# Performance work log

Measured on AMD Instinct MI355X. Metric: run time of the kernel, lower is better.

The kernel has to match this reference:

```python
import jax, jax.numpy as jnp
import numpy as np

P = 1024
D_FF = 4096
TGT = 4096
SRC = 4096


def _ln(x, g, b, eps=1e-5):
    mu = jnp.mean(x, axis=-1, keepdims=True)
    var = jnp.mean((x - mu) ** 2, axis=-1, keepdims=True)
    return (x - mu) / jnp.sqrt(var + eps) * g + b


def setup_inputs() -> dict:
    key = jax.random.key(0)
    ks = jax.random.split(key, 32)
    s = 1.0 / np.sqrt(P)
    sf = 1.0 / np.sqrt(D_FF)
    d = {
        "Y": jax.random.normal(ks[0], (TGT, P), jnp.float32),
        "Xp": jax.random.normal(ks[1], (SRC, P), jnp.float32),
        # self-attn projections (Linear: y = x @ W + b, W stored [in, out])
        "wq1": jax.random.uniform(ks[2], (P, P), jnp.float32, -s, s),
        "bq1": jnp.zeros((P,), jnp.float32),
        "wk1": jax.random.uniform(ks[3], (P, P), jnp.float32, -s, s),
        "bk1": jnp.zeros((P,), jnp.float32),
        "wv1": jax.random.uniform(ks[4], (P, P), jnp.float32, -s, s),
        "bv1": jnp.zeros((P,), jnp.float32),
        "w0": jax.random.uniform(ks[5], (P, P), jnp.float32, -s, s),
        "b0": jnp.zeros((P,), jnp.float32),
        "g1": jnp.ones((P,), jnp.float32),
        "be1": jnp.zeros((P,), jnp.float32),
        # cross-attn projections
        "wq2": jax.random.uniform(ks[6], (P, P), jnp.float32, -s, s),
        "bq2": jnp.zeros((P,), jnp.float32),
        "wk2": jax.random.uniform(ks[7], (P, P), jnp.float32, -s, s),
        "bk2": jnp.zeros((P,), jnp.float32),
        "wv2": jax.random.uniform(ks[8], (P, P), jnp.float32, -s, s),
        "bv2": jnp.zeros((P,), jnp.float32),
        "w1": jax.random.uniform(ks[9], (P, P), jnp.float32, -s, s),
        "b1": jnp.zeros((P,), jnp.float32),
        "g2": jnp.ones((P,), jnp.float32),
        "be2": jnp.zeros((P,), jnp.float32),
        # FFN
        "w2": jax.random.uniform(ks[10], (P, D_FF), jnp.float32, -s, s),
        "b2": jnp.zeros((D_FF,), jnp.float32),
        "w3": jax.random.uniform(ks[11], (D_FF, P), jnp.float32, -sf, sf),
        "b3": jnp.zeros((P,), jnp.float32),
        "g3": jnp.ones((P,), jnp.float32),
        "be3": jnp.zeros((P,), jnp.float32),
    }
    return d


def reference(Y, Xp, wq1, bq1, wk1, bk1, wv1, bv1, w0, b0, g1, be1,
              wq2, bq2, wk2, bk2, wv2, bv2, w1, b1, g2, be2,
              w2, b2, w3, b3, g3, be3):
    m = Y.shape[0]
    scale = 1.0 / jnp.sqrt(jnp.asarray(P, Y.dtype))
    # --- masked self-attention on Y ---
    Q = Y @ wq1 + bq1            # [m, p]
    K = Y @ wk1 + bk1
    V = Y @ wv1 + bv1
    S = (Q @ K.T) * scale        # [m, m]
    causal = jnp.tril(jnp.ones((m, m), bool))
    S = jnp.where(causal, S, jnp.asarray(-1e9, S.dtype))
    A = jax.nn.softmax(S, axis=-1)
    T1 = (A @ V) @ w0 + b0
    U1 = _ln(Y + T1, g1, be1)
    # --- cross-attention with encoder output Xp ---
    Q = U1 @ wq2 + bq2           # [m, p]
    K = Xp @ wk2 + bk2           # [n, p]
    V = Xp @ wv2 + bv2
    S = (Q @ K.T) * scale        # [m, n]
    A = jax.nn.softmax(S, axis=-1)
    T2 = (A @ V) @ w1 + b1
    U2 = _ln(U1 + T2, g2, be2)
    # --- position-wise FFN ---
    Z = jax.nn.relu(U2 @ w2 + b2) @ w3 + b3
    U3 = _ln(U2 + Z, g3, be3)
    return U3
```

## Files before the change

kernel.cpp:

```cpp
#include <hip/hip_runtime.h>
#include <hip/hip_bf16.h>

typedef __bf16 bf16x8 __attribute__((ext_vector_type(8)));
typedef __bf16 bf16x4 __attribute__((ext_vector_type(4)));
typedef float f32x4 __attribute__((ext_vector_type(4)));

#define AS1P(p) ((__attribute__((address_space(1))) void*)(void*)(p))
#define AS3P(p) ((__attribute__((address_space(3))) void*)(p))

__global__ __launch_bounds__(256, 3) void gemm_bt(
    const __hip_bfloat16* __restrict__ A, int lda,
    const __hip_bfloat16* __restrict__ Bt, int ldb,
    int M, int N, int K, int ldc,
    const float* __restrict__ bias, int bias_mode,
    float scale,
    const float* __restrict__ residual,
    int relu, int causal_skip, int trapezoid, int ksplit,
    float* __restrict__ Cf, __hip_bfloat16* __restrict__ Cb,
    int vcol0, __hip_bfloat16* __restrict__ Vt, int ldvt,
    int nsplit1, const __hip_bfloat16* __restrict__ A2,
    const __hip_bfloat16* __restrict__ Bt2, int ldb2, int ldc2,
    const float* __restrict__ bias2, __hip_bfloat16* __restrict__ Cb2,
    int vcol0_2, __hip_bfloat16* __restrict__ Vt2, int ldvt2)
{
    int nb = blockIdx.x;
    int mb = blockIdx.y;
    {
        const int gx = gridDim.x, gy = gridDim.y;
        if ((gx & 3) == 0 && (gy & 1) == 0) {
            const int id = mb * gx + nb;
            const int X  = id & 7;
            const int L  = id >> 3;
            const int rn = gx >> 2, rm = gy >> 1;
            const int nb_l = L / rm, mb_l = L - nb_l * rm;
            nb = (X & 3) * rn + nb_l;
            mb = (X >> 2) * rm + mb_l;
        }
    }
    if (nsplit1 && nb >= nsplit1) {
        A = A2; Bt = Bt2; ldb = ldb2; ldc = ldc2; bias = bias2;
        Cb = Cb2; Cf = nullptr; residual = nullptr;
        vcol0 = vcol0_2; Vt = Vt2; ldvt = ldvt2;
        nb -= nsplit1;
    }
    const int m_base = mb * 128;
    const int n_base = nb * 128;
    if (causal_skip && (n_base > m_base + 127)) return;
    int Kend = K;
    if (trapezoid) { int kl = m_base + 128; Kend = kl < K ? kl : K; }
    int kb = 0, ke = Kend;
    if (ksplit) {
        kb = blockIdx.z * ksplit;
        int k2 = kb + ksplit; ke = k2 < Kend ? k2 : Kend;
        if (kb >= ke) return;
        Cb += (size_t)blockIdx.z * M * ldc;
        Cf = nullptr;
    }
    const int nt = (ke - kb) >> 5;

    __shared__ __align__(16) __hip_bfloat16 Lds[3][8192];

    const int tid  = threadIdx.x;
    const int lane = tid & 63;
    const int wave = tid >> 6;
    const int wm = (wave >> 1) * 64;
    const int wn = (wave & 1) * 64;

    f32x4 acc[4][4];
#pragma unroll
    for (int i = 0; i < 4; ++i)
#pragma unroll
        for (int j = 0; j < 4; ++j) acc[i][j] = f32x4{0.f, 0.f, 0.f, 0.f};

    const bool isA = wave < 2;
    const __hip_bfloat16* G = isA ? (A + (size_t)m_base * lda) : (Bt + (size_t)n_base * ldb);
    const int ldg = isA ? lda : ldb;
    const int q0 = (wave & 1) * 4;
    const int rsub = lane >> 2;
    const int cx   = (lane & 3) ^ ((lane >> 3) & 3);
    const size_t grow = (size_t)(q0 * 16 + rsub) * ldg + (size_t)cx * 8 + kb;
    const int ldsoff = (isA ? 0 : 4096) + q0 * 512;

    const int lrow = lane & 15;
    const int cph  = ((lane >> 4) ^ ((lrow >> 1) & 3)) * 8;

#define ISSUE_TILE(KT, STG)                                                      \
    {                                                                            \
        const __hip_bfloat16* g = G + grow + (size_t)(KT) * 32;                  \
        __hip_bfloat16* dst = &Lds[STG][ldsoff];                                 \
        _Pragma("unroll")                                                        \
        for (int q = 0; q < 4; ++q) {                                            \
            __builtin_amdgcn_global_load_lds(AS1P(g), AS3P(dst), 16, 0, 0);      \
            g += (size_t)16 * ldg; dst += 512;                                   \
        }                                                                        \
    }

    ISSUE_TILE(0, 0)
    if (nt > 1) ISSUE_TILE(1, 1)

    int cur = 0;
    for (int kt = 0; kt < nt; ++kt) {
        __builtin_amdgcn_sched_barrier(0);
        if (kt + 1 < nt) __builtin_amdgcn_s_waitcnt(0x0F74);
        else             __builtin_amdgcn_s_waitcnt(0x0F70);
        __builtin_amdgcn_sched_barrier(0);
        __builtin_amdgcn_s_barrier();
        __builtin_amdgcn_sched_barrier(0);
        if (kt + 2 < nt) {
            int s2 = cur + 2; if (s2 >= 3) s2 -= 3;
            ISSUE_TILE(kt + 2, s2)
        }

        bf16x8 af[4], bfv[4];
#pragma unroll
        for (int i = 0; i < 4; ++i)
            af[i] = *(const bf16x8*)&Lds[cur][(wm + i * 16 + lrow) * 32 + cph];
#pragma unroll
        for (int j = 0; j < 4; ++j)
            bfv[j] = *(const bf16x8*)&Lds[cur][4096 + (wn + j * 16 + lrow) * 32 + cph];
#pragma unroll
        for (int i = 0; i < 4; ++i)
#pragma unroll
            for (int j = 0; j < 4; ++j)
                acc[i][j] = __builtin_amdgcn_mfma_f32_16x16x32_bf16(af[i], bfv[j], acc[i][j], 0, 0, 0);

        cur = (cur + 1 == 3) ? 0 : cur + 1;
    }
#undef ISSUE_TILE

    const int r0 = (lane >> 4) * 4;
    const int c0 = lane & 15;
    const bool vtrans = (n_base >= vcol0);
#pragma unroll
    for (int i = 0; i < 4; ++i) {
#pragma unroll
        for (int j = 0; j < 4; ++j) {
            const int col = n_base + wn + j * 16 + c0;
            const int row0 = m_base + wm + i * 16 + r0;
            float vv[4];
#pragma unroll
            for (int r = 0; r < 4; ++r) {
                float v = acc[i][j][r] * scale;
                if (bias_mode == 1) v += bias[col];
                else if (bias_mode == 2) v += bias[row0 + r];
                if (relu) v = fmaxf(v, 0.f);
                vv[r] = v;
            }
            if (vtrans) {
                bf16x4 o = { (__bf16)vv[0], (__bf16)vv[1], (__bf16)vv[2], (__bf16)vv[3] };
                *(bf16x4*)(Vt + (size_t)(col - vcol0) * ldvt + row0) = o;
            } else {
#pragma unroll
                for (int r = 0; r < 4; ++r) {
                    const size_t idx = (size_t)(row0 + r) * ldc + col;
                    float v = vv[r];
                    if (residual) v += residual[idx];
                    if (Cf) Cf[idx] = v;
                    else    Cb[idx] = __float2bfloat16(v);
                }
            }
        }
    }
}

__global__ __launch_bounds__(256, 2) void gemm_bt2(
    const __hip_bfloat16* __restrict__ A, int lda,
    const __hip_bfloat16* __restrict__ Bt, int ldb,
    int M, int N, int K, int ldc,
    const float* __restrict__ bias, int bias_mode,
    float scale,
    int relu, int causal_skip, int trapezoid, int ksplit,
    __hip_bfloat16* __restrict__ Cb)
{
    int nb = blockIdx.x;
    int mb = blockIdx.y;
    {
        const int gx = gridDim.x, gy = gridDim.y;
        if ((gx & 3) == 0 && (gy & 1) == 0) {
            const int id = mb * gx + nb;
            const int X  = id & 7;
            const int L  = id >> 3;
            const int rn = gx >> 2, rm = gy >> 1;
            const int nb_l = L / rm, mb_l = L - nb_l * rm;
            nb = (X & 3) * rn + nb_l;
            mb = (X >> 2) * rm + mb_l;
        }
    }
    const int m_base = mb * 256;
    const int n_base = nb * 128;
    if (causal_skip && (n_base > m_base + 255)) return;
    int Kend = K;
    if (trapezoid) { int kl = m_base + 256; Kend = kl < K ? kl : K; }
    int kb = 0, ke = Kend;
    if (ksplit) {
        kb = blockIdx.z * ksplit;
        int k2 = kb + ksplit; ke = k2 < Kend ? k2 : Kend;
        if (kb >= ke) return;
        Cb += (size_t)blockIdx.z * M * ldc;
    }
    const int nt = (ke - kb) >> 5;

    __shared__ __align__(16) __hip_bfloat16 Lds[3][12288];

    const int tid  = threadIdx.x;
    const int lane = tid & 63;
    const int wave = tid >> 6;
    const int wtm = (wave >> 1) * 128;
    const int wtn = (wave & 1) * 64;

    f32x4 acc[8][4];
#pragma unroll
    for (int i = 0; i < 8; ++i)
#pragma unroll
        for (int j = 0; j < 4; ++j) acc[i][j] = f32x4{0.f, 0.f, 0.f, 0.f};

    const int rsub = lane >> 2;
    const int cx   = (lane & 3) ^ ((lane >> 3) & 3);
    const __hip_bfloat16* GA = A  + (size_t)(m_base + wave * 64) * lda + (size_t)rsub * lda + (size_t)cx * 8 + kb;
    const __hip_bfloat16* GB = Bt + (size_t)(n_base + wave * 32) * ldb + (size_t)rsub * ldb + (size_t)cx * 8 + kb;
    const int ldsA = wave * 2048;
    const int ldsB = 8192 + wave * 1024;

    const int lrow = lane & 15;
    const int cph  = ((lane >> 4) ^ ((lrow >> 1) & 3)) * 8;

#define ISSUE_TILE2(KT, STG)                                                     \
    {                                                                            \
        const size_t ko = (size_t)(KT) * 32;                                     \
        const __hip_bfloat16* ga = GA + ko;                                      \
        __hip_bfloat16* da = &Lds[STG][ldsA];                                    \
        _Pragma("unroll")                                                        \
        for (int q = 0; q < 4; ++q) {                                            \
            __builtin_amdgcn_global_load_lds(AS1P(ga), AS3P(da), 16, 0, 0);      \
            ga += (size_t)16 * lda; da += 512;                                   \
        }                                                                        \
        const __hip_bfloat16* gb = GB + ko;                                      \
        __hip_bfloat16* db = &Lds[STG][ldsB];                                    \
        _Pragma("unroll")                                                        \
        for (int q = 0; q < 2; ++q) {                                            \
            __builtin_amdgcn_global_load_lds(AS1P(gb), AS3P(db), 16, 0, 0);      \
            gb += (size_t)16 * ldb; db += 512;                                   \
        }                                                                        \
    }

    ISSUE_TILE2(0, 0)
    if (nt > 1) ISSUE_TILE2(1, 1)

    int cur = 0;
    for (int kt = 0; kt < nt; ++kt) {
        __builtin_amdgcn_sched_barrier(0);
        if (kt + 1 < nt) __builtin_amdgcn_s_waitcnt(0x0F76);
        else             __builtin_amdgcn_s_waitcnt(0x0F70);
        __builtin_amdgcn_sched_barrier(0);
        __builtin_amdgcn_s_barrier();
        __builtin_amdgcn_sched_barrier(0);
        if (kt + 2 < nt) {
            int s2 = cur + 2; if (s2 >= 3) s2 -= 3;
            ISSUE_TILE2(kt + 2, s2)
        }

        bf16x8 af[8], bfv[4];
#pragma unroll
        for (int i = 0; i < 8; ++i)
            af[i] = *(const bf16x8*)&Lds[cur][(wtm + i * 16 + lrow) * 32 + cph];
#pragma unroll
        for (int j = 0; j < 4; ++j)
            bfv[j] = *(const bf16x8*)&Lds[cur][8192 + (wtn + j * 16 + lrow) * 32 + cph];
#pragma unroll
        for (int i = 0; i < 8; ++i)
#pragma unroll
            for (int j = 0; j < 4; ++j)
                acc[i][j] = __builtin_amdgcn_mfma_f32_16x16x32_bf16(af[i], bfv[j], acc[i][j], 0, 0, 0);

        cur = (cur + 1 == 3) ? 0 : cur + 1;
    }
#undef ISSUE_TILE2

    const int r0 = (lane >> 4) * 4;
    const int c0 = lane & 15;
#pragma unroll
    for (int i = 0; i < 8; ++i) {
#pragma unroll
        for (int j = 0; j < 4; ++j) {
            const int col = n_base + wtn + j * 16 + c0;
#pragma unroll
            for (int r = 0; r < 4; ++r) {
                const int row = m_base + wtm + i * 16 + r0 + r;
                float v = acc[i][j][r] * scale;
                if (bias_mode == 1) v += bias[col];
                else if (bias_mode == 2) v += bias[row];
                if (relu) v = fmaxf(v, 0.f);
                Cb[(size_t)row * ldc + col] = __float2bfloat16(v);
            }
        }
    }
}

__global__ __launch_bounds__(256) void reduce_k_kernel(
    const __hip_bfloat16* __restrict__ Pb, int M, int N, int nsplit, int KC, int trapK,
    const float* __restrict__ bias, const float* __restrict__ residual,
    float* __restrict__ Cf, __hip_bfloat16* __restrict__ Cb)
{
    const int idx = blockIdx.x * 256 + threadIdx.x;
    const int nv = N >> 2;
    const int row = idx / nv;
    if (row >= M) return;
    const int c4 = (idx - row * nv) * 4;
    int nc = nsplit;
    if (trapK) {
        int kend = (row & ~255) + 256; if (kend > trapK) kend = trapK;
        nc = (kend + KC - 1) / KC;
    }
    float s0 = 0.f, s1 = 0.f, s2 = 0.f, s3 = 0.f;
    for (int c = 0; c < nc; ++c) {
        const bf16x4 p = *(const bf16x4*)(Pb + ((size_t)c * M + row) * N + c4);
        s0 += (float)p[0]; s1 += (float)p[1]; s2 += (float)p[2]; s3 += (float)p[3];
    }
    if (bias) {
        const f32x4 b = *(const f32x4*)(bias + c4);
        s0 += b[0]; s1 += b[1]; s2 += b[2]; s3 += b[3];
    }
    if (residual) {
        const f32x4 rv = *(const f32x4*)(residual + (size_t)row * N + c4);
        s0 += rv[0]; s1 += rv[1]; s2 += rv[2]; s3 += rv[3];
    }
    if (Cf) { f32x4 o = {s0, s1, s2, s3}; *(f32x4*)(Cf + (size_t)row * N + c4) = o; }
    else {
        bf16x4 o = { (__bf16)s0, (__bf16)s1, (__bf16)s2, (__bf16)s3 };
        *(bf16x4*)(Cb + (size_t)row * N + c4) = o;
    }
}

__global__ __launch_bounds__(256) void reduce_ln_kernel(
    const __hip_bfloat16* __restrict__ Pb, int M, int nsplit,
    const float* __restrict__ bias, const float* __restrict__ residual,
    const float* __restrict__ g, const float* __restrict__ b,
    float* __restrict__ outF, __hip_bfloat16* __restrict__ outB)
{
    __shared__ float sm[8];
    const int row = blockIdx.x;
    const int tid = threadIdx.x;
    const int c4 = tid * 4;

    float v0 = 0.f, v1 = 0.f, v2 = 0.f, v3 = 0.f;
    for (int c = 0; c < nsplit; ++c) {
        const bf16x4 p = *(const bf16x4*)(Pb + ((size_t)c * M + row) * 1024 + c4);
        v0 += (float)p[0]; v1 += (float)p[1]; v2 += (float)p[2]; v3 += (float)p[3];
    }
    {
        const f32x4 bv = *(const f32x4*)(bias + c4);
        v0 += bv[0]; v1 += bv[1]; v2 += bv[2]; v3 += bv[3];
    }
    {
        const f32x4 rv = *(const f32x4*)(residual + (size_t)row * 1024 + c4);
        v0 += rv[0]; v1 += rv[1]; v2 += rv[2]; v3 += rv[3];
    }

    float s  = v0 + v1 + v2 + v3;
    float ss = v0 * v0 + v1 * v1 + v2 * v2 + v3 * v3;
#pragma unroll
    for (int o = 32; o; o >>= 1) { s += __shfl_down(s, o); ss += __shfl_down(ss, o); }
    if ((tid & 63) == 0) { sm[tid >> 6] = s; sm[4 + (tid >> 6)] = ss; }
    __syncthreads();
    s  = sm[0] + sm[1] + sm[2] + sm[3];
    ss = sm[4] + sm[5] + sm[6] + sm[7];
    const float mu   = s * (1.f / 1024.f);
    const float var  = ss * (1.f / 1024.f) - mu * mu;
    const float rstd = rsqrtf(var + 1e-5f);
    const float4 gv = ((const float4*)g)[tid];
    const float4 bv = ((const float4*)b)[tid];
    float4 o;
    o.x = (v0 - mu) * rstd * gv.x + bv.x;
    o.y = (v1 - mu) * rstd * gv.y + bv.y;
    o.z = (v2 - mu) * rstd * gv.z + bv.z;
    o.w = (v3 - mu) * rstd * gv.w + bv.w;
    ((float4*)(outF + (size_t)row * 1024))[tid] = o;
    if (outB) {
        bf16x4 ob = { (__bf16)o.x, (__bf16)o.y, (__bf16)o.z, (__bf16)o.w };
        *(bf16x4*)(outB + (size_t)row * 1024 + c4) = ob;
    }
}

struct PrepTab {
    const float* src[12];
    __hip_bfloat16* dst[12];
    int K[12];
    int N[12];
    int trans[12];
    int blk0[13];
};

__global__ __launch_bounds__(256) void prep_kernel(PrepTab t)
{
    __shared__ float tile[32][33];
    const int bid = blockIdx.x;
    int e = 0;
    while (e < 11 && bid >= t.blk0[e + 1]) ++e;
    const int local = bid - t.blk0[e];
    const int N = t.N[e];
    const int K = t.K[e];
    const int ntx = N >> 5;
    const int n0 = (local % ntx) * 32;
    const int k0 = (local / ntx) * 32;
    const float* __restrict__ W = t.src[e];
    __hip_bfloat16* __restrict__ D = t.dst[e];
    const int tx = threadIdx.x;
    const int ty = threadIdx.y;
    if (t.trans[e]) {
        for (int i = ty; i < 32; i += 8)
            tile[i][tx] = W[(size_t)(k0 + i) * N + n0 + tx];
        __syncthreads();
        for (int i = ty; i < 32; i += 8)
            D[(size_t)(n0 + i) * K + k0 + tx] = __float2bfloat16(tile[tx][i]);
    } else {
        for (int i = ty; i < 32; i += 8) {
            const size_t idx = (size_t)(k0 + i) * N + n0 + tx;
            D[idx] = __float2bfloat16(W[idx]);
        }
    }
}

__global__ __launch_bounds__(256) void bias_pack_kernel(
    const float* __restrict__ bq1, const float* __restrict__ bk1,
    const float* __restrict__ bv1, const float* __restrict__ bk2,
    const float* __restrict__ bv2, float* __restrict__ bqkv1,
    float* __restrict__ bkv2)
{
    const int i = blockIdx.x * 256 + threadIdx.x;
    if (i < 1024)       bqkv1[i] = bq1[i];
    else if (i < 2048)  bqkv1[i] = bk1[i - 1024];
    else if (i < 3072)  bqkv1[i] = bv1[i - 2048];
    else if (i < 4096)  bkv2[i - 3072] = bk2[i - 3072];
    else if (i < 5120)  bkv2[i - 3072] = bv2[i - 4096];
}

__global__ __launch_bounds__(256) void softmax_kernel(
    const __hip_bfloat16* __restrict__ S, __hip_bfloat16* __restrict__ A, int N, int causal)
{
    __shared__ float sm[4];
    const int row = blockIdx.x;
    const int tid = threadIdx.x;
    const int limit = causal ? (row + 1) : N;
    const int zl0 = (row & ~255) + 256;
    const int zlimit = causal ? (zl0 < N ? zl0 : N) : N;
    const __hip_bfloat16* Srow = S + (size_t)row * N;
    __hip_bfloat16* Arow = A + (size_t)row * N;

    float x[4][4];
    float m = -3.0e38f;
#pragma unroll
    for (int p = 0; p < 4; ++p) {
        const int cb = p * 1024 + tid * 4;
        if (cb < limit) {
            const bf16x4 xv = *(const bf16x4*)(Srow + cb);
#pragma unroll
            for (int e = 0; e < 4; ++e) {
                const float f = (cb + e < limit) ? (float)xv[e] : -3.0e38f;
                x[p][e] = f;
                m = fmaxf(m, f);
            }
        } else {
#pragma unroll
            for (int e = 0; e < 4; ++e) x[p][e] = -3.0e38f;
        }
    }
#pragma unroll
    for (int o = 32; o; o >>= 1) m = fmaxf(m, __shfl_down(m, o));
    if ((tid & 63) == 0) sm[tid >> 6] = m;
    __syncthreads();
    m = fmaxf(fmaxf(sm[0], sm[1]), fmaxf(sm[2], sm[3]));
    __syncthreads();

    float s = 0.f;
#pragma unroll
    for (int p = 0; p < 4; ++p) {
        const int cb = p * 1024 + tid * 4;
        if (cb < limit) {
#pragma unroll
            for (int e = 0; e < 4; ++e) {
                const float ev = (cb + e < limit) ? __expf(x[p][e] - m) : 0.f;
                x[p][e] = ev;
                s += ev;
            }
        } else {
#pragma unroll
            for (int e = 0; e < 4; ++e) x[p][e] = 0.f;
        }
    }
#pragma unroll
    for (int o = 32; o; o >>= 1) s += __shfl_down(s, o);
    if ((tid & 63) == 0) sm[tid >> 6] = s;
    __syncthreads();
    s = sm[0] + sm[1] + sm[2] + sm[3];
    const float inv = 1.f / s;

#pragma unroll
    for (int p = 0; p < 4; ++p) {
        const int cb = p * 1024 + tid * 4;
        if (cb < zlimit) {
            bf16x4 o = { (__bf16)(x[p][0] * inv), (__bf16)(x[p][1] * inv),
                         (__bf16)(x[p][2] * inv), (__bf16)(x[p][3] * inv) };
            *(bf16x4*)(Arow + cb) = o;
        }
    }
}

extern "C" void kernel_launch(void* const* d_in, const int* in_sizes, int n_in,
                              void* d_out, int out_size, void* d_ws, size_t ws_size,
                              hipStream_t stream)
{
    const int M = 4096, Pd = 1024, DFF = 4096, NS = 4096;
    const size_t MB = 1024 * 1024;
    const int NOV = 0x40000000;

    const float* Y   = (const float*)d_in[0];
    const float* Xp  = (const float*)d_in[1];
    const float* wq1 = (const float*)d_in[2];  const float* bq1 = (const float*)d_in[3];
    const float* wk1 = (const float*)d_in[4];  const float* bk1 = (const float*)d_in[5];
    const float* wv1 = (const float*)d_in[6];  const float* bv1 = (const float*)d_in[7];
    const float* w0  = (const float*)d_in[8];  const float* b0  = (const float*)d_in[9];
    const float* g1  = (const float*)d_in[10]; const float* be1 = (const float*)d_in[11];
    const float* wq2 = (const float*)d_in[12]; const float* bq2 = (const float*)d_in[13];
    const float* wk2 = (const float*)d_in[14]; const float* bk2 = (const float*)d_in[15];
    const float* wv2 = (const float*)d_in[16]; const float* bv2 = (const float*)d_in[17];
    const float* w1  = (const float*)d_in[18]; const float* b1  = (const float*)d_in[19];
    const float* g2  = (const float*)d_in[20]; const float* be2 = (const float*)d_in[21];
    const float* w2  = (const float*)d_in[22]; const float* b2  = (const float*)d_in[23];
    const float* w3  = (const float*)d_in[24]; const float* b3  = (const float*)d_in[25];
    const float* g3  = (const float*)d_in[26]; const float* be3 = (const float*)d_in[27];

    char* ws = (char*)d_ws;
    __hip_bfloat16* Ybf   = (__hip_bfloat16*)(ws + 0 * MB);
    __hip_bfloat16* Ubf   = (__hip_bfloat16*)(ws + 0 * MB);
    __hip_bfloat16* Xpbf  = (__hip_bfloat16*)(ws + 8 * MB);
    __hip_bfloat16* AVbf  = (__hip_bfloat16*)(ws + 8 * MB);
    __hip_bfloat16* Qbf   = (__hip_bfloat16*)(ws + 8 * MB);
    __hip_bfloat16* wqkv1t= (__hip_bfloat16*)(ws + 16 * MB);
    __hip_bfloat16* w0t   = (__hip_bfloat16*)(ws + 22 * MB);
    __hip_bfloat16* wq2t  = (__hip_bfloat16*)(ws + 24 * MB);
    __hip_bfloat16* wkv2t = (__hip_bfloat16*)(ws + 26 * MB);
    __hip_bfloat16* w1t   = (__hip_bfloat16*)(ws + 30 * MB);
    __hip_bfloat16* w2t   = (__hip_bfloat16*)(ws + 32 * MB);
    __hip_bfloat16* w3t   = (__hip_bfloat16*)(ws + 40 * MB);
    float*          bqkv1 = (float*)(ws + 48 * MB);
    float*          bkv2  = (float*)(ws + 48 * MB + 512 * 1024);
    __hip_bfloat16* QKV1  = (__hip_bfloat16*)(ws + 49 * MB);
    __hip_bfloat16* KV2   = (__hip_bfloat16*)(ws + 73 * MB);
    __hip_bfloat16* Vt1   = (__hip_bfloat16*)(ws + 89 * MB);
    __hip_bfloat16* Sb    = (__hip_bfloat16*)(ws + 97 * MB);
    __hip_bfloat16* Pb    = (__hip_bfloat16*)(ws + 97 * MB);
    __hip_bfloat16* Abf   = (__hip_bfloat16*)(ws + 161 * MB);
    __hip_bfloat16* Vt2   = (__hip_bfloat16*)(ws + 193 * MB);
    float*          Uf    = (float*)(ws + 209 * MB);
    float*          Out   = (float*)d_out;
    if (ws_size < 225 * MB) return;

    auto gemm = [&](const __hip_bfloat16* A, int lda, const __hip_bfloat16* Bt, int ldb,
                    int Mm, int Nn, int Kk, int ldc,
                    const float* bias, int bmode, float scale, const float* res,
                    int relu, int causal, int trap, int ksplit,
                    float* Cf, __hip_bfloat16* Cb) {
        const int nz = ksplit ? (Kk + ksplit - 1) / ksplit : 1;
        gemm_bt<<<dim3(Nn / 128, Mm / 128, nz), dim3(256), 0, stream>>>(
            A, lda, Bt, ldb, Mm, Nn, Kk, ldc, bias, bmode, scale, res, relu, causal, trap, ksplit,
            Cf, Cb, NOV, nullptr, 0,
            0, nullptr, nullptr, 0, 0, nullptr, nullptr, NOV, nullptr, 0);
    };
    auto gemm2 = [&](const __hip_bfloat16* A, int lda, const __hip_bfloat16* Bt, int ldb,
                     int Mm, int Nn, int Kk, int ldc,
                     const float* bias, int bmode, float scale,
                     int relu, int causal, int trap, int ksplit, __hip_bfloat16* Cb) {
        const int nz = ksplit ? (Kk + ksplit - 1) / ksplit : 1;
        gemm_bt2<<<dim3(Nn / 128, Mm / 256, nz), dim3(256), 0, stream>>>(
            A, lda, Bt, ldb, Mm, Nn, Kk, ldc, bias, bmode, scale, relu, causal, trap, ksplit, Cb);
    };
    auto reduce = [&](const __hip_bfloat16* P, int Mm, int Nn, int nsplit, int KC, int trapK,
                      const float* bias, const float* res, float* Cf, __hip_bfloat16* Cb) {
        reduce_k_kernel<<<dim3(Mm * Nn / 1024), dim3(256), 0, stream>>>(
            P, Mm, Nn, nsplit, KC, trapK, bias, res, Cf, Cb);
    };
    auto reduce_ln = [&](const __hip_bfloat16* P, int nsplit,
                         const float* bias, const float* res,
                         const float* gg, const float* bb,
                         float* outF, __hip_bfloat16* outB) {
        reduce_ln_kernel<<<dim3(M), dim3(256), 0, stream>>>(
            P, M, nsplit, bias, res, gg, bb, outF, outB);
    };

    const float scl = 0.03125f;

    {
        PrepTab t;
        const float* srcs[12]  = { wq1, wk1, wv1, w0, wq2, wk2, wv2, w1, w2, w3, Y, Xp };
        __hip_bfloat16* dsts[12] = { wqkv1t, wqkv1t + Pd * Pd, wqkv1t + 2 * Pd * Pd,
                                     w0t, wq2t, wkv2t, wkv2t + Pd * Pd, w1t,
                                     w2t, w3t, Ybf, Xpbf };
        const int Ks[12] = { Pd, Pd, Pd, Pd, Pd, Pd, Pd, Pd, Pd,  DFF, M,  NS };
        const int Ns[12] = { Pd, Pd, Pd, Pd, Pd, Pd, Pd, Pd, DFF, Pd,  Pd, Pd };
        const int trs[12] = { 1, 1, 1, 1, 1, 1, 1, 1, 1, 1, 0, 0 };
        int acc = 0;
        for (int e = 0; e < 12; ++e) {
            t.src[e] = srcs[e]; t.dst[e] = dsts[e];
            t.K[e] = Ks[e]; t.N[e] = Ns[e]; t.trans[e] = trs[e];
            t.blk0[e] = acc;
            acc += (Ns[e] / 32) * (Ks[e] / 32);
        }
        t.blk0[12] = acc;
        prep_kernel<<<dim3(acc), dim3(32, 8), 0, stream>>>(t);
    }
    bias_pack_kernel<<<dim3(20), dim3(256), 0, stream>>>(bq1, bk1, bv1, bk2, bv2, bqkv1, bkv2);

    gemm_bt<<<dim3(40, 32, 1), dim3(256), 0, stream>>>(
        Ybf, Pd, wqkv1t, Pd, M, 3072, Pd, 3072, bqkv1, 1, 1.f, nullptr, 0, 0, 0, 0,
        nullptr, QKV1, 2048, Vt1, M,
        24, Xpbf, wkv2t, Pd, 2048, bkv2, KV2, 1024, Vt2, NS);

    gemm2(QKV1, 3072, QKV1 + 1024, 3072, M, M, Pd, M,
          nullptr, 0, scl, 0, 1, 0, 0, Sb);
    softmax_kernel<<<dim3(M), dim3(256), 0, stream>>>(Sb, Abf, M, 1);
    gemm2(Abf, M, Vt1, M, M, Pd, M, Pd,
          nullptr, 0, 1.f, 0, 0, 1, 1024, Pb);
    reduce(Pb, M, Pd, 4, 1024, M, nullptr, nullptr, nullptr, AVbf);
    gemm(AVbf, Pd, w0t, Pd, M, Pd, Pd, Pd,
         nullptr, 0, 1.f, nullptr, 0, 0, 0, 512, nullptr, Pb);
    reduce_ln(Pb, 2, b0, Y, g1, be1, Uf, Ubf);

    gemm(Ubf, Pd, wq2t, Pd, M, Pd, Pd, Pd,
         nullptr, 0, 1.f, nullptr, 0, 0, 0, 512, nullptr, Pb);
    reduce(Pb, M, Pd, 2, 512, 0, bq2, nullptr, nullptr, Qbf);
    gemm2(Qbf, Pd, KV2, 2048, M, NS, Pd, NS,
          nullptr, 0, scl, 0, 0, 0, 0, Sb);
    softmax_kernel<<<dim3(M), dim3(256), 0, stream>>>(Sb, Abf, NS, 0);
    gemm2(Abf, NS, Vt2, NS, M, Pd, NS, Pd,
          nullptr, 0, 1.f, 0, 0, 0, 1024, Pb);
    reduce(Pb, M, Pd, 4, 1024, 0, nullptr, nullptr, nullptr, AVbf);
    gemm(AVbf, Pd, w1t, Pd, M, Pd, Pd, Pd,
         nullptr, 0, 1.f, nullptr, 0, 0, 0, 512, nullptr, Pb);
    reduce_ln(Pb, 2, b1, Uf, g2, be2, Uf, Ubf);

    gemm2(Ubf, Pd, w2t, Pd, M, DFF, Pd, DFF, b2, 1, 1.f, 1, 0, 0, 0, Abf);
    gemm2(Abf, DFF, w3t, DFF, M, Pd, DFF, Pd,
          nullptr, 0, 1.f, 0, 0, 0, 1024, Pb);
    reduce_ln(Pb, 4, b3, Uf, g3, be3, Out, nullptr);
}
```

Baseline: 679.4 us.

## Add 256x256-tile 8-wave GEMM for cross-attention and FFN matmuls

Adds gemm_bt3, a 512-thread GEMM with 256x256 output tiles, a triple-buffered LDS pipeline and a grouped block-index swizzle. It replaces the 256x128 gemm_bt2 for the cross-attention QK^T and AV products and both FFN matmuls. The larger tile doubles operand reuse per LDS load and lowers global traffic per FLOP. The trade-off is more LDS per block (96KB) and higher register pressure, which likely limits each CU to a single resident block.

```diff
diff --git a/kernel.cpp b/kernel.cpp
--- a/kernel.cpp
+++ b/kernel.cpp
@@ -275,6 +275,139 @@
         cur = (cur + 1 == 3) ? 0 : cur + 1;
     }
 #undef ISSUE_TILE2
+
+    const int r0 = (lane >> 4) * 4;
+    const int c0 = lane & 15;
+#pragma unroll
+    for (int i = 0; i < 8; ++i) {
+#pragma unroll
+        for (int j = 0; j < 4; ++j) {
+            const int col = n_base + wtn + j * 16 + c0;
+#pragma unroll
+            for (int r = 0; r < 4; ++r) {
+                const int row = m_base + wtm + i * 16 + r0 + r;
+                float v = acc[i][j][r] * scale;
+                if (bias_mode == 1) v += bias[col];
+                else if (bias_mode == 2) v += bias[row];
+                if (relu) v = fmaxf(v, 0.f);
+                Cb[(size_t)row * ldc + col] = __float2bfloat16(v);
+            }
+        }
+    }
+}
+
+__global__ __launch_bounds__(512, 2) void gemm_bt3(
+    const __hip_bfloat16* __restrict__ A, int lda,
+    const __hip_bfloat16* __restrict__ Bt, int ldb,
+    int M, int N, int K, int ldc,
+    const float* __restrict__ bias, int bias_mode,
+    float scale,
+    int relu, int causal_skip, int trapezoid, int ksplit,
+    __hip_bfloat16* __restrict__ Cb)
+{
+    int nb = blockIdx.x;
+    int mb = blockIdx.y;
+    {
+        const int gx = gridDim.x, gy = gridDim.y;
+        if ((gx & 3) == 0 && (gy & 1) == 0) {
+            const int id = mb * gx + nb;
+            const int X  = id & 7;
+            const int L  = id >> 3;
+            const int rn = gx >> 2, rm = gy >> 1;
+            const int nb_l = L / rm, mb_l = L - nb_l * rm;
+            nb = (X & 3) * rn + nb_l;
+            mb = (X >> 2) * rm + mb_l;
+        }
+    }
+    const int m_base = mb * 256;
+    const int n_base = nb * 256;
+    if (causal_skip && (n_base > m_base + 255)) return;
+    int Kend = K;
+    if (trapezoid) { int kl = m_base + 256; Kend = kl < K ? kl : K; }
+    int kb = 0, ke = Kend;
+    if (ksplit) {
+        kb = blockIdx.z * ksplit;
+        int k2 = kb + ksplit; ke = k2 < Kend ? k2 : Kend;
+        if (kb >= ke) return;
+        Cb += (size_t)blockIdx.z * M * ldc;
+    }
+    const int nt = (ke - kb) >> 5;
+
+    __shared__ __align__(16) __hip_bfloat16 Lds[3][16384];
+
+    const int tid  = threadIdx.x;
+    const int lane = tid & 63;
+    const int wave = tid >> 6;
+    const int wtm = (wave >> 2) * 128;
+    const int wtn = (wave & 3) * 64;
+
+    f32x4 acc[8][4];
+#pragma unroll
+    for (int i = 0; i < 8; ++i)
+#pragma unroll
+        for (int j = 0; j < 4; ++j) acc[i][j] = f32x4{0.f, 0.f, 0.f, 0.f};
+
+    const int rsub = lane >> 2;
+    const int cx   = (lane & 3) ^ ((lane >> 3) & 3);
+    const __hip_bfloat16* GA = A  + (size_t)(m_base + wave * 32 + rsub) * lda + (size_t)cx * 8 + kb;
+    const __hip_bfloat16* GB = Bt + (size_t)(n_base + wave * 32 + rsub) * ldb + (size_t)cx * 8 + kb;
+    const int ldsA = wave * 1024;
+    const int ldsB = 8192 + wave * 1024;
+
+    const int lrow = lane & 15;
+    const int cph  = ((lane >> 4) ^ ((lrow >> 1) & 3)) * 8;
+
+#define ISSUE_TILE3(KT, STG)                                                     \
+    {                                                                            \
+        const size_t ko = (size_t)(KT) * 32;                                     \
+        const __hip_bfloat16* ga = GA + ko;                                      \
+        __hip_bfloat16* da = &Lds[STG][ldsA];                                    \
+        _Pragma("unroll")                                                        \
+        for (int q = 0; q < 2; ++q) {                                            \
+            __builtin_amdgcn_global_load_lds(AS1P(ga), AS3P(da), 16, 0, 0);      \
+            ga += (size_t)16 * lda; da += 512;                                   \
+        }                                                                        \
+        const __hip_bfloat16* gb = GB + ko;                                      \
+        __hip_bfloat16* db = &Lds[STG][ldsB];                                    \
+        _Pragma("unroll")                                                        \
+        for (int q = 0; q < 2; ++q) {                                            \
+            __builtin_amdgcn_global_load_lds(AS1P(gb), AS3P(db), 16, 0, 0);      \
+            gb += (size_t)16 * ldb; db += 512;                                   \
+        }                                                                        \
+    }
+
+    ISSUE_TILE3(0, 0)
+    if (nt > 1) ISSUE_TILE3(1, 1)
+
+    int cur = 0;
+    for (int kt = 0; kt < nt; ++kt) {
+        __builtin_amdgcn_sched_barrier(0);
+        if (kt + 1 < nt) __builtin_amdgcn_s_waitcnt(0x0F74);
+        else             __builtin_amdgcn_s_waitcnt(0x0F70);
+        __builtin_amdgcn_sched_barrier(0);
+        __builtin_amdgcn_s_barrier();
+        __builtin_amdgcn_sched_barrier(0);
+        if (kt + 2 < nt) {
+            int s2 = cur + 2; if (s2 >= 3) s2 -= 3;
+            ISSUE_TILE3(kt + 2, s2)
+        }
+
+        bf16x8 af[8], bfv[4];
+#pragma unroll
+        for (int i = 0; i < 8; ++i)
+            af[i] = *(const bf16x8*)&Lds[cur][(wtm + i * 16 + lrow) * 32 + cph];
+#pragma unroll
+        for (int j = 0; j < 4; ++j)
+            bfv[j] = *(const bf16x8*)&Lds[cur][8192 + (wtn + j * 16 + lrow) * 32 + cph];
+#pragma unroll
+        for (int i = 0; i < 8; ++i)
+#pragma unroll
+            for (int j = 0; j < 4; ++j)
+                acc[i][j] = __builtin_amdgcn_mfma_f32_16x16x32_bf16(af[i], bfv[j], acc[i][j], 0, 0, 0);
+
+        cur = (cur + 1 == 3) ? 0 : cur + 1;
+    }
+#undef ISSUE_TILE3
 
     const int r0 = (lane >> 4) * 4;
     const int c0 = lane & 15;
@@ -574,6 +707,14 @@
         gemm_bt2<<<dim3(Nn / 128, Mm / 256, nz), dim3(256), 0, stream>>>(
             A, lda, Bt, ldb, Mm, Nn, Kk, ldc, bias, bmode, scale, relu, causal, trap, ksplit, Cb);
     };
+    auto gemm3 = [&](const __hip_bfloat16* A, int lda, const __hip_bfloat16* Bt, int ldb,
+                     int Mm, int Nn, int Kk, int ldc,
+                     const float* bias, int bmode, float scale,
+                     int relu, int causal, int trap, int ksplit, __hip_bfloat16* Cb) {
+        const int nz = ksplit ? (Kk + ksplit - 1) / ksplit : 1;
+        gemm_bt3<<<dim3(Nn / 256, Mm / 256, nz), dim3(512), 0, stream>>>(
+            A, lda, Bt, ldb, Mm, Nn, Kk, ldc, bias, bmode, scale, relu, causal, trap, ksplit, Cb);
+    };
     auto reduce = [&](const __hip_bfloat16* P, int Mm, int Nn, int nsplit, int KC, int trapK,
                       const float* bias, const float* res, float* Cf, __hip_bfloat16* Cb) {
         reduce_k_kernel<<<dim3(Mm * Nn / 1024), dim3(256), 0, stream>>>(
@@ -628,18 +769,18 @@
     gemm(Ubf, Pd, wq2t, Pd, M, Pd, Pd, Pd,
          nullptr, 0, 1.f, nullptr, 0, 0, 0, 512, nullptr, Pb);
     reduce(Pb, M, Pd, 2, 512, 0, bq2, nullptr, nullptr, Qbf);
-    gemm2(Qbf, Pd, KV2, 2048, M, NS, Pd, NS,
+    gemm3(Qbf, Pd, KV2, 2048, M, NS, Pd, NS,
           nullptr, 0, scl, 0, 0, 0, 0, Sb);
     softmax_kernel<<<dim3(M), dim3(256), 0, stream>>>(Sb, Abf, NS, 0);
-    gemm2(Abf, NS, Vt2, NS, M, Pd, NS, Pd,
+    gemm3(Abf, NS, Vt2, NS, M, Pd, NS, Pd,
           nullptr, 0, 1.f, 0, 0, 0, 1024, Pb);
     reduce(Pb, M, Pd, 4, 1024, 0, nullptr, nullptr, nullptr, AVbf);
     gemm(AVbf, Pd, w1t, Pd, M, Pd, Pd, Pd,
          nullptr, 0, 1.f, nullptr, 0, 0, 0, 512, nullptr, Pb);
     reduce_ln(Pb, 2, b1, Uf, g2, be2, Uf, Ubf);
 
-    gemm2(Ubf, Pd, w2t, Pd, M, DFF, Pd, DFF, b2, 1, 1.f, 1, 0, 0, 0, Abf);
-    gemm2(Abf, DFF, w3t, DFF, M, Pd, DFF, Pd,
+    gemm3(Ubf, Pd, w2t, Pd, M, DFF, Pd, DFF, b2, 1, 1.f, 1, 0, 0, 0, Abf);
+    gemm3(Abf, DFF, w3t, DFF, M, Pd, DFF, Pd,
           nullptr, 0, 1.f, 0, 0, 0, 1024, Pb);
     reduce_ln(Pb, 4, b3, Uf, g3, be3, Out, nullptr);
 }
```

Result: no change. 668.4 us, median of 2 (-1.6%).
